# Performance work log

Measured on AMD Instinct MI355X. Metric: run time of the kernel, lower is better.

The kernel has to match this reference:

```python
import jax, jax.numpy as jnp
import numpy as np

B, N, D, H = 8, 8192, 512, 8  # batch, seq, hidden, heads
DH = D // H


def _rope_tables(n, d, dtype=jnp.float32):
    # standard rotate-half RoPE tables over the full hidden dim (d/2 freq pairs)
    half = d // 2
    inv_freq = 1.0 / (10000.0 ** (np.arange(0, half, dtype=np.float32) / half))
    pos = np.arange(n, dtype=np.float32)
    ang = np.einsum('n,f->nf', pos, inv_freq)          # [N, D/2]
    ang = np.concatenate([ang, ang], axis=-1)          # [N, D]
    return jnp.asarray(np.cos(ang), dtype), jnp.asarray(np.sin(ang), dtype)


def setup_inputs() -> dict:
    key = jax.random.key(0)
    k1, k2 = jax.random.split(key)
    hidden_states = jax.random.normal(k1, (B, N, D), dtype=jnp.float32)
    num_layers = 24
    std = 0.02 / np.sqrt(2.0 * num_layers * D)
    W = jax.random.normal(k2, (D, D), dtype=jnp.float32) * std
    cos, sin = _rope_tables(N, D)
    return {"hidden_states": hidden_states, "W": W, "cos": cos, "sin": sin}


def _rotate_half(x):
    x1, x2 = jnp.split(x, 2, axis=-1)
    return jnp.concatenate([-x2, x1], axis=-1)


def reference(hidden_states, W, cos, sin):
    # dropout(p=0) in eval mode -> identity
    x = hidden_states * cos + _rotate_half(hidden_states) * sin  # RoPE, [B,N,D]
    q = jnp.einsum('bnd,ed->bne', x, W)                          # F.linear(x, W)
    qh = q.reshape(B, N, H, DH)
    xh = x.reshape(B, N, H, DH)
    # linear-complexity path: (K^T V) then Q @ (.), per head
    kv = jnp.einsum('bnhd,bnhe->bhde', xh, xh)   # [B,H,DH,DH]
    out = jnp.einsum('bnhd,bhde->bnhe', qh, kv)  # [B,N,H,DH]
    return out.reshape(B, N, D)
```

## Files before the change

### kernel.cpp

```cpp
#include <hip/hip_runtime.h>
#include <hip/hip_bf16.h>
#include <stdint.h>

#define BB 8
#define NN 8192
#define DD 512
#define HH 8
#define DHD 64
#define NCH 32

typedef __attribute__((ext_vector_type(8))) short bf16x8;
typedef __attribute__((ext_vector_type(4))) float f32x4;
typedef __attribute__((ext_vector_type(4))) float f4v;

__device__ __forceinline__ unsigned short f2bf(float f) {
  union { float f; unsigned int u; } v; v.f = f;
  return (unsigned short)((v.u + 0x7FFFu + ((v.u >> 16) & 1u)) >> 16);
}

__device__ __forceinline__ void async16(const void* g, void* l) {
  __builtin_amdgcn_global_load_lds(
      (const __attribute__((address_space(1))) void*)g,
      (__attribute__((address_space(3))) void*)l, 16, 0, 0);
}

__global__ __launch_bounds__(512, 2) void ropekv_kernel(
    const float* __restrict__ h, const float* __restrict__ cs,
    const float* __restrict__ sn, unsigned short* __restrict__ x,
    float* __restrict__ kvp, int nbh) {
  __shared__ __align__(16) unsigned int xt32[512 * 34];
  int blk = blockIdx.x;
  int chunk = blk & 31, b = blk >> 5;
  int tid = threadIdx.x;
  int wave = tid >> 6, lane = tid & 63;
  int rpar = lane & 1;
  int g = lane >> 1;
  int cf = g * 8;
  int l15 = lane & 15, q = lane >> 4;
  int hd = wave * 64;
  size_t row0 = (size_t)b * NN + (size_t)chunk * 256;
  int n0 = chunk * 256;

  f32x4 acc[4][4];
#pragma unroll
  for (int i = 0; i < 4; ++i)
#pragma unroll
    for (int j = 0; j < 4; ++j) acc[i][j] = (f32x4){0.f, 0.f, 0.f, 0.f};

  f4v ha[4][2], hbv[4][2];

  auto loadt = [&](int t) {
#pragma unroll
    for (int p = 0; p < 4; ++p) {
      int r = p * 16 + wave * 2 + rpar;
      const float* hp = h + (row0 + t * 64 + r) * DD + cf;
      ha[p][0]  = __builtin_nontemporal_load((const f4v*)hp);
      ha[p][1]  = __builtin_nontemporal_load((const f4v*)(hp + 4));
      hbv[p][0] = __builtin_nontemporal_load((const f4v*)(hp + 256));
      hbv[p][1] = __builtin_nontemporal_load((const f4v*)(hp + 260));
    }
  };

  auto ropet = [&](int t) {
#pragma unroll
    for (int p = 0; p < 4; ++p) {
      int r = p * 16 + wave * 2 + rpar;
      int nr = n0 + t * 64 + r;
      const float* cp = cs + (size_t)nr * DD + cf;
      const float* sp = sn + (size_t)nr * DD + cf;
      f4v c0 = *(const f4v*)cp, c1 = *(const f4v*)(cp + 4);
      f4v s0 = *(const f4v*)sp, s1 = *(const f4v*)(sp + 4);
      f4v xl0 = ha[p][0] * c0 - hbv[p][0] * s0;
      f4v xl1 = ha[p][1] * c1 - hbv[p][1] * s1;
      f4v xh0 = hbv[p][0] * c0 + ha[p][0] * s0;
      f4v xh1 = hbv[p][1] * c1 + ha[p][1] * s1;
      unsigned ml[4], mh[4];
      ml[0] = (unsigned)f2bf(xl0.x) | ((unsigned)f2bf(xl0.y) << 16);
      ml[1] = (unsigned)f2bf(xl0.z) | ((unsigned)f2bf(xl0.w) << 16);
      ml[2] = (unsigned)f2bf(xl1.x) | ((unsigned)f2bf(xl1.y) << 16);
      ml[3] = (unsigned)f2bf(xl1.z) | ((unsigned)f2bf(xl1.w) << 16);
      mh[0] = (unsigned)f2bf(xh0.x) | ((unsigned)f2bf(xh0.y) << 16);
      mh[1] = (unsigned)f2bf(xh0.z) | ((unsigned)f2bf(xh0.w) << 16);
      mh[2] = (unsigned)f2bf(xh1.x) | ((unsigned)f2bf(xh1.y) << 16);
      mh[3] = (unsigned)f2bf(xh1.z) | ((unsigned)f2bf(xh1.w) << 16);
      unsigned short* xp = x + (row0 + t * 64 + r) * DD + cf;
      uint4 st0; st0.x = ml[0]; st0.y = ml[1]; st0.z = ml[2]; st0.w = ml[3];
      uint4 st1; st1.x = mh[0]; st1.y = mh[1]; st1.z = mh[2]; st1.w = mh[3];
      *(uint4*)xp         = st0;
      *(uint4*)(xp + 256) = st1;
      unsigned pk[8];
#pragma unroll
      for (int k = 0; k < 4; ++k) {
        unsigned mine = rpar ? mh[k] : ml[k];
        unsigned send = rpar ? ml[k] : mh[k];
        unsigned recv = (unsigned)__shfl_xor((int)send, 1, 64);
        if (!rpar) {
          pk[2 * k]     = (mine & 0xffffu) | (recv << 16);
          pk[2 * k + 1] = (mine >> 16) | (recv & 0xffff0000u);
        } else {
          pk[2 * k]     = (recv & 0xffffu) | (mine << 16);
          pk[2 * k + 1] = (recv >> 16) | (mine & 0xffff0000u);
        }
      }
      int np = p * 8 + wave;
      int dbase = cf + (rpar ? 256 : 0);
      int rot = (g >> 1) & 7;
#pragma unroll
      for (int w = 0; w < 8; ++w) {
        int jj = (w + rot) & 7;
        xt32[(dbase + jj) * 34 + np] = pk[jj];
      }
    }
  };

  loadt(0);
  for (int t = 0; t < 4; ++t) {
    ropet(t);
    __syncthreads();
    if (t < 3) loadt(t + 1);
    const unsigned short* xt16 = (const unsigned short*)xt32;
#pragma unroll
    for (int ks = 0; ks < 64; ks += 32) {
      bf16x8 af[4];
#pragma unroll
      for (int i = 0; i < 4; ++i)
        af[i] = *(const bf16x8*)&xt16[(hd + i * 16 + l15) * 68 + ks + q * 8];
#pragma unroll
      for (int i = 0; i < 4; ++i)
#pragma unroll
        for (int j = 0; j < 4; ++j)
          acc[i][j] = __builtin_amdgcn_mfma_f32_16x16x32_bf16(af[i], af[j], acc[i][j], 0, 0, 0);
    }
    __syncthreads();
  }

  int bh = b * 8 + wave;
  float* dst = kvp + ((size_t)chunk * nbh + bh) * 4096;
#pragma unroll
  for (int i = 0; i < 4; ++i)
#pragma unroll
    for (int j = 0; j < 4; ++j)
#pragma unroll
      for (int reg = 0; reg < 4; ++reg)
        dst[(i * 16 + q * 4 + reg) * 64 + j * 16 + l15] = acc[i][j][reg];
}

__global__ __launch_bounds__(512, 2) void wkvt_kernel(
    const float* __restrict__ W, const float* __restrict__ kvp,
    unsigned short* __restrict__ wkvt, int nbh) {
  __shared__ float kvs[64 * 16];
  __shared__ __align__(16) float ws[64 * 512];
  int blk = blockIdx.x;
  int bh = blk >> 2, eq = blk & 3;
  int b = bh >> 3, hh = bh & 7;
  int tid = threadIdx.x;
  if (tid < 256) {
    int idx = tid * 4;
    int d = idx >> 4, ec = idx & 15;
    f4v s = (f4v){0.f, 0.f, 0.f, 0.f};
    for (int c = 0; c < NCH; ++c)
      s += *(const f4v*)&kvp[((size_t)c * nbh + bh) * 4096 + d * 64 + eq * 16 + ec];
    *(f4v*)&kvs[idx] = s;
  }
#pragma unroll
  for (int i = 0; i < 16; ++i) {
    int idx = i * 2048 + tid * 4;
    *(f4v*)&ws[idx] = *(const f4v*)&W[(size_t)(hh * DHD + (idx >> 9)) * DD + (idx & 511)];
  }
  __syncthreads();
  int el = tid & 15, fg = tid >> 4;
  f4v av[4];
#pragma unroll
  for (int k = 0; k < 4; ++k) av[k] = (f4v){0.f, 0.f, 0.f, 0.f};
#pragma unroll 8
  for (int d = 0; d < 64; ++d) {
    float kvv = kvs[d * 16 + el];
    const f4v* wr = (const f4v*)&ws[d * DD + fg * 16];
#pragma unroll
    for (int k = 0; k < 4; ++k) av[k] += wr[k] * kvv;
  }
  unsigned short tb[16];
#pragma unroll
  for (int k = 0; k < 4; ++k) {
    tb[k * 4 + 0] = f2bf(av[k].x); tb[k * 4 + 1] = f2bf(av[k].y);
    tb[k * 4 + 2] = f2bf(av[k].z); tb[k * 4 + 3] = f2bf(av[k].w);
  }
  size_t ob = ((size_t)b * DD + hh * DHD + eq * 16 + el) * DD + fg * 16;
  *(uint4*)&wkvt[ob]     = *(uint4*)&tb[0];
  *(uint4*)&wkvt[ob + 8] = *(uint4*)&tb[8];
}

__global__ __launch_bounds__(256, 2) void gemm_kernel(const unsigned short* __restrict__ x,
                                                      const unsigned short* __restrict__ wkvt,
                                                      float* __restrict__ out) {
  __shared__ __align__(16) unsigned short As[128 * 64];
  __shared__ __align__(16) unsigned short Bs[256 * 64];
  int mt = blockIdx.x, ct = blockIdx.y, bz = blockIdx.z;
  int tid = threadIdx.x, wave = tid >> 6, lane = tid & 63;
  int m_off = (wave & 1) * 64, c_off = (wave >> 1) * 128;
  int l15 = lane & 15, q = lane >> 4;
  int lrow = lane >> 3, lcol = (lane & 7) * 8;
  const unsigned short* Ag = x    + ((size_t)bz * NN + mt * 128) * DD;
  const unsigned short* Bg = wkvt + ((size_t)bz * DD + ct * 256) * DD;
  f32x4 acc[4][8];
#pragma unroll
  for (int i = 0; i < 4; ++i)
#pragma unroll
    for (int j = 0; j < 8; ++j) acc[i][j] = (f32x4){0.f, 0.f, 0.f, 0.f};

  for (int kk = 0; kk < 512; kk += 64) {
#pragma unroll
    for (int i = 0; i < 4; ++i)
      async16(Ag + (size_t)(wave * 32 + i * 8 + lrow) * DD + kk + lcol,
              &As[(wave * 32 + i * 8) * 64]);
#pragma unroll
    for (int i = 0; i < 8; ++i)
      async16(Bg + (size_t)(wave * 64 + i * 8 + lrow) * DD + kk + lcol,
              &Bs[(wave * 64 + i * 8) * 64]);
    __syncthreads();
#pragma unroll
    for (int ks = 0; ks < 64; ks += 32) {
      bf16x8 a[4], bb[8];
#pragma unroll
      for (int i = 0; i < 4; ++i)
        a[i] = *(const bf16x8*)&As[(m_off + i * 16 + l15) * 64 + ks + q * 8];
#pragma unroll
      for (int j = 0; j < 8; ++j)
        bb[j] = *(const bf16x8*)&Bs[(c_off + j * 16 + l15) * 64 + ks + q * 8];
#pragma unroll
      for (int i = 0; i < 4; ++i)
#pragma unroll
        for (int j = 0; j < 8; ++j)
          acc[i][j] = __builtin_amdgcn_mfma_f32_16x16x32_bf16(a[i], bb[j], acc[i][j], 0, 0, 0);
    }
    __syncthreads();
  }
  float* ob = out + ((size_t)bz * NN + mt * 128) * DD + ct * 256;
#pragma unroll
  for (int i = 0; i < 4; ++i)
#pragma unroll
    for (int j = 0; j < 8; ++j) {
      int row = m_off + i * 16 + q * 4;
      int col = c_off + j * 16 + l15;
#pragma unroll
      for (int reg = 0; reg < 4; ++reg)
        __builtin_nontemporal_store(acc[i][j][reg], &ob[(size_t)(row + reg) * DD + col]);
    }
}

extern "C" void kernel_launch(void* const* d_in, const int* in_sizes, int n_in,
                              void* d_out, int out_size, void* d_ws, size_t ws_size,
                              hipStream_t stream) {
  (void)in_sizes; (void)n_in; (void)out_size;
  const float* h  = (const float*)d_in[0];
  const float* W  = (const float*)d_in[1];
  const float* cs = (const float*)d_in[2];
  const float* sn = (const float*)d_in[3];
  float* out = (float*)d_out;

  const size_t x_full     = (size_t)BB * NN * DD * 2;
  const size_t kvp_full   = (size_t)NCH * BB * HH * DHD * DHD * 4;
  const size_t wkvt_full  = (size_t)BB * DD * DD * 2;
  const size_t x_batch    = (size_t)NN * DD * 2;
  const size_t kvp_batch  = (size_t)NCH * HH * DHD * DHD * 4;
  const size_t wkvt_batch = (size_t)DD * DD * 2;

  if (ws_size >= x_full + kvp_full + wkvt_full) {
    unsigned short* xw   = (unsigned short*)d_ws;
    float*          kvp  = (float*)((char*)d_ws + x_full);
    unsigned short* wkvt = (unsigned short*)((char*)d_ws + x_full + kvp_full);
    ropekv_kernel<<<dim3(BB * 32), dim3(512), 0, stream>>>(h, cs, sn, xw, kvp, BB * HH);
    wkvt_kernel<<<dim3(BB * HH * 4), dim3(512), 0, stream>>>(W, kvp, wkvt, BB * HH);
    gemm_kernel<<<dim3(NN / 128, DD / 256, BB), dim3(256), 0, stream>>>(xw, wkvt, out);
  } else {
    unsigned short* xw   = (unsigned short*)d_ws;
    float*          kvp  = (float*)((char*)d_ws + x_batch);
    unsigned short* wkvt = (unsigned short*)((char*)d_ws + x_batch + kvp_batch);
    for (int b = 0; b < BB; ++b) {
      ropekv_kernel<<<dim3(32), dim3(512), 0, stream>>>(
          h + (size_t)b * NN * DD, cs, sn, xw, kvp, HH);
      wkvt_kernel<<<dim3(HH * 4), dim3(512), 0, stream>>>(W, kvp, wkvt, HH);
      gemm_kernel<<<dim3(NN / 128, DD / 256, 1), dim3(256), 0, stream>>>(
          xw, wkvt, out + (size_t)b * NN * DD);
    }
  }
}
```

Measured before the change: 336.0 us.

## Rewrite GEMM as 256x256 tile, 8-wave, double-buffered pipelined kernel

The GEMM kernel moves from 128x256 tiles with 4 waves and a single LDS buffer to 256x256 tiles with 8 waves. LDS is split into double-buffered halves, and async global-to-LDS loads for future k-steps are interleaved with MFMA work using explicit vmcnt waits, barriers and setprio. LDS is XOR-swizzled to avoid bank conflicts, and the 1D grid is remapped to a chiplet-aware block order. The aim is to hide memory latency and improve operand reuse, at the cost of a more fragile hand-scheduled pipeline and lower occupancy from the larger LDS and register footprint.

Result: no change. 331.0 us (-1.5%).

```diff
diff --git a/kernel.cpp b/kernel.cpp
--- a/kernel.cpp
+++ b/kernel.cpp
@@ -190,62 +190,128 @@
   *(uint4*)&wkvt[ob + 8] = *(uint4*)&tb[8];
 }
 
-__global__ __launch_bounds__(256, 2) void gemm_kernel(const unsigned short* __restrict__ x,
+constexpr int c_stM[8] = {0, 1, 0, 1, 0, 1, 0, 1};
+constexpr int c_stP[8] = {1, 1, 0, 0, 0, 0, 1, 1};
+constexpr int c_stH[8] = {1, 1, 0, 0, 1, 1, 0, 0};
+constexpr int c_stO[8] = {1, 1, 2, 2, 2, 2, 3, 3};
+
+__global__ __launch_bounds__(512, 2) void gemm_kernel(const unsigned short* __restrict__ x,
                                                       const unsigned short* __restrict__ wkvt,
                                                       float* __restrict__ out) {
-  __shared__ __align__(16) unsigned short As[128 * 64];
-  __shared__ __align__(16) unsigned short Bs[256 * 64];
-  int mt = blockIdx.x, ct = blockIdx.y, bz = blockIdx.z;
+  __shared__ __align__(16) unsigned short Ab[2][2][128 * 64];
+  __shared__ __align__(16) unsigned short Bb[2][2][128 * 64];
+  int u = blockIdx.x;
+  int cpx = gridDim.x >> 3;
+  int l = (u & 7) * cpx + (u >> 3);
+  int ct = l & 1, mt = (l >> 1) & 31, bz = l >> 6;
   int tid = threadIdx.x, wave = tid >> 6, lane = tid & 63;
-  int m_off = (wave & 1) * 64, c_off = (wave >> 1) * 128;
+  int wm = wave & 1, wn = wave >> 1;
   int l15 = lane & 15, q = lane >> 4;
-  int lrow = lane >> 3, lcol = (lane & 7) * 8;
-  const unsigned short* Ag = x    + ((size_t)bz * NN + mt * 128) * DD;
+  const unsigned short* Ag = x    + ((size_t)bz * NN + mt * 256) * DD;
   const unsigned short* Bg = wkvt + ((size_t)bz * DD + ct * 256) * DD;
-  f32x4 acc[4][8];
-#pragma unroll
-  for (int i = 0; i < 4; ++i)
-#pragma unroll
-    for (int j = 0; j < 8; ++j) acc[i][j] = (f32x4){0.f, 0.f, 0.f, 0.f};
-
-  for (int kk = 0; kk < 512; kk += 64) {
-#pragma unroll
-    for (int i = 0; i < 4; ++i)
-      async16(Ag + (size_t)(wave * 32 + i * 8 + lrow) * DD + kk + lcol,
-              &As[(wave * 32 + i * 8) * 64]);
-#pragma unroll
-    for (int i = 0; i < 8; ++i)
-      async16(Bg + (size_t)(wave * 64 + i * 8 + lrow) * DD + kk + lcol,
-              &Bs[(wave * 64 + i * 8) * 64]);
-    __syncthreads();
-#pragma unroll
-    for (int ks = 0; ks < 64; ks += 32) {
-      bf16x8 a[4], bb[8];
-#pragma unroll
-      for (int i = 0; i < 4; ++i)
-        a[i] = *(const bf16x8*)&As[(m_off + i * 16 + l15) * 64 + ks + q * 8];
-#pragma unroll
-      for (int j = 0; j < 8; ++j)
-        bb[j] = *(const bf16x8*)&Bs[(c_off + j * 16 + l15) * 64 + ks + q * 8];
-#pragma unroll
-      for (int i = 0; i < 4; ++i)
-#pragma unroll
-        for (int j = 0; j < 8; ++j)
-          acc[i][j] = __builtin_amdgcn_mfma_f32_16x16x32_bf16(a[i], bb[j], acc[i][j], 0, 0, 0);
-    }
-    __syncthreads();
-  }
-  float* ob = out + ((size_t)bz * NN + mt * 128) * DD + ct * 256;
-#pragma unroll
-  for (int i = 0; i < 4; ++i)
+
+  int row0 = tid >> 3,         ss0 = (tid & 7) ^ (row0 & 7);
+  int row1 = (512 + tid) >> 3, ss1 = ((512 + tid) & 7) ^ (row1 & 7);
+  const unsigned short* At0 = Ag + (size_t)row0 * DD + ss0 * 8;
+  const unsigned short* At1 = Ag + (size_t)row1 * DD + ss1 * 8;
+  const unsigned short* Bt0 = Bg + (size_t)row0 * DD + ss0 * 8;
+  const unsigned short* Bt1 = Bg + (size_t)row1 * DD + ss1 * 8;
+
+  auto stgA = [&](int P, int hf, int kt) {
+    async16(At0 + (size_t)hf * 128 * DD + kt * 64, &Ab[P][hf][wave * 512]);
+    async16(At1 + (size_t)hf * 128 * DD + kt * 64, &Ab[P][hf][4096 + wave * 512]);
+  };
+  auto stgB = [&](int P, int hf, int kt) {
+    async16(Bt0 + (size_t)hf * 128 * DD + kt * 64, &Bb[P][hf][wave * 512]);
+    async16(Bt1 + (size_t)hf * 128 * DD + kt * 64, &Bb[P][hf][4096 + wave * 512]);
+  };
+
+  int sw0 = ((q ^ (l15 & 7)) << 3);
+  int sw1 = (((4 + q) ^ (l15 & 7)) << 3);
+
+  bf16x8 Ar[4][2], Br[4][2];
+  auto loadA4 = [&](int P, int a) {
+#pragma unroll
+    for (int f = 0; f < 4; ++f) {
+      int r = (a * 64 + f * 16 + l15) * 64;
+      Ar[f][0] = *(const bf16x8*)&Ab[P][wm][r + sw0];
+      Ar[f][1] = *(const bf16x8*)&Ab[P][wm][r + sw1];
+    }
+  };
+  auto loadB2 = [&](int P, int n0) {
+#pragma unroll
+    for (int f = 0; f < 2; ++f) {
+      int r = ((wn & 1) * 64 + (n0 + f) * 16 + l15) * 64;
+      Br[n0 + f][0] = *(const bf16x8*)&Bb[P][wn >> 1][r + sw0];
+      Br[n0 + f][1] = *(const bf16x8*)&Bb[P][wn >> 1][r + sw1];
+    }
+  };
+
+  f32x4 acc[8][4];
+#pragma unroll
+  for (int i = 0; i < 8; ++i)
+#pragma unroll
+    for (int j = 0; j < 4; ++j) acc[i][j] = (f32x4){0.f, 0.f, 0.f, 0.f};
+
+  stgB(0, 0, 0); stgA(0, 0, 0); stgB(0, 1, 0); stgA(0, 1, 0);
+  stgB(1, 0, 1); stgA(1, 0, 1);
+  asm volatile("s_waitcnt vmcnt(4)" ::: "memory");
+  __builtin_amdgcn_s_barrier();
+
+#pragma unroll
+  for (int i = 0; i < 4; ++i) {
 #pragma unroll
     for (int j = 0; j < 8; ++j) {
-      int row = m_off + i * 16 + q * 4;
-      int col = c_off + j * 16 + l15;
-#pragma unroll
-      for (int reg = 0; reg < 4; ++reg)
-        __builtin_nontemporal_store(acc[i][j][reg], &ob[(size_t)(row + reg) * DD + col]);
-    }
+      constexpr int jm[8] = {0, 1, 0, 1, 0, 1, 0, 1};
+      (void)jm;
+      int P = j >> 2;
+      int a = (j >> 1) & 1;
+      int b2 = (j & 1) * 2;
+      if ((j & 3) == 0) loadB2(P, 0);
+      if ((j & 3) == 1) loadB2(P, 2);
+      if ((j & 1) == 0) loadA4(P, a);
+      if (2 * i + c_stO[j] < 8) {
+        if (c_stM[j]) stgA(c_stP[j], c_stH[j], 2 * i + c_stO[j]);
+        else          stgB(c_stP[j], c_stH[j], 2 * i + c_stO[j]);
+      }
+      __builtin_amdgcn_s_barrier();
+      asm volatile("s_waitcnt lgkmcnt(0)" ::: "memory");
+      __builtin_amdgcn_sched_barrier(0);
+      __builtin_amdgcn_s_setprio(1);
+#pragma unroll
+      for (int f = 0; f < 4; ++f)
+#pragma unroll
+        for (int nn = 0; nn < 2; ++nn) {
+          acc[a * 4 + f][b2 + nn] = __builtin_amdgcn_mfma_f32_16x16x32_bf16(
+              Ar[f][0], Br[b2 + nn][0], acc[a * 4 + f][b2 + nn], 0, 0, 0);
+          acc[a * 4 + f][b2 + nn] = __builtin_amdgcn_mfma_f32_16x16x32_bf16(
+              Ar[f][1], Br[b2 + nn][1], acc[a * 4 + f][b2 + nn], 0, 0, 0);
+        }
+      __builtin_amdgcn_s_setprio(0);
+      if (i == 3 && j == 3) {
+        asm volatile("s_waitcnt vmcnt(0)" ::: "memory");
+      } else if ((j & 3) == 3) {
+        asm volatile("s_waitcnt vmcnt(4)" ::: "memory");
+      }
+      __builtin_amdgcn_s_barrier();
+    }
+  }
+
+  float* ob = out + ((size_t)bz * NN + mt * 256 + wm * 128) * DD + ct * 256 + wn * 64;
+#pragma unroll
+  for (int f = 0; f < 4; ++f) {
+#pragma unroll
+    for (int a = 0; a < 2; ++a)
+#pragma unroll
+      for (int nn = 0; nn < 4; ++nn) {
+        int row = a * 64 + f * 16 + q * 4;
+        int col = nn * 16 + l15;
+#pragma unroll
+        for (int reg = 0; reg < 4; ++reg)
+          __builtin_nontemporal_store(acc[a * 4 + f][nn][reg],
+                                      &ob[(size_t)(row + reg) * DD + col]);
+      }
+  }
 }
 
 extern "C" void kernel_launch(void* const* d_in, const int* in_sizes, int n_in,
@@ -271,7 +337,7 @@
     unsigned short* wkvt = (unsigned short*)((char*)d_ws + x_full + kvp_full);
     ropekv_kernel<<<dim3(BB * 32), dim3(512), 0, stream>>>(h, cs, sn, xw, kvp, BB * HH);
     wkvt_kernel<<<dim3(BB * HH * 4), dim3(512), 0, stream>>>(W, kvp, wkvt, BB * HH);
-    gemm_kernel<<<dim3(NN / 128, DD / 256, BB), dim3(256), 0, stream>>>(xw, wkvt, out);
+    gemm_kernel<<<dim3((NN / 256) * (DD / 256) * BB), dim3(512), 0, stream>>>(xw, wkvt, out);
   } else {
     unsigned short* xw   = (unsigned short*)d_ws;
     float*          kvp  = (float*)((char*)d_ws + x_batch);
@@ -280,7 +346,7 @@
       ropekv_kernel<<<dim3(32), dim3(512), 0, stream>>>(
           h + (size_t)b * NN * DD, cs, sn, xw, kvp, HH);
       wkvt_kernel<<<dim3(HH * 4), dim3(512), 0, stream>>>(W, kvp, wkvt, HH);
-      gemm_kernel<<<dim3(NN / 128, DD / 256, 1), dim3(256), 0, stream>>>(
+      gemm_kernel<<<dim3((NN / 256) * (DD / 256)), dim3(512), 0, stream>>>(
           xw, wkvt, out + (size_t)b * NN * DD);
     }
   }
```

## Double-buffer LDS tile and register prefetch in RoPE/KV kernel pipeline

Applied to the files above, without the earlier changes.

The kernel now keeps two LDS transpose buffers and two register sets for the loaded hidden-state tiles. The loop is software-pipelined: loads run two tiles ahead and RoPE runs one tile ahead of the MFMA accumulation, which drops one barrier per iteration. The aim is to overlap global loads and RoPE ALU work with the matrix ops. In exchange, LDS per block roughly doubles (about 139KB), which may not fit two blocks per CU. The extra register buffers also raise register pressure under launch_bounds(512,2).

New measurement: 336.0 us. About the same (+0.0%).

```diff
diff --git a/kernel.cpp b/kernel.cpp
--- a/kernel.cpp
+++ b/kernel.cpp
@@ -28,7 +28,7 @@
     const float* __restrict__ h, const float* __restrict__ cs,
     const float* __restrict__ sn, unsigned short* __restrict__ x,
     float* __restrict__ kvp, int nbh) {
-  __shared__ __align__(16) unsigned int xt32[512 * 34];
+  __shared__ __align__(16) unsigned int xt32[2][512 * 34];
   int blk = blockIdx.x;
   int chunk = blk & 31, b = blk >> 5;
   int tid = threadIdx.x;
@@ -47,21 +47,23 @@
 #pragma unroll
     for (int j = 0; j < 4; ++j) acc[i][j] = (f32x4){0.f, 0.f, 0.f, 0.f};
 
-  f4v ha[4][2], hbv[4][2];
+  f4v ha[2][4][2], hb[2][4][2];
 
   auto loadt = [&](int t) {
+    int pb = t & 1;
 #pragma unroll
     for (int p = 0; p < 4; ++p) {
       int r = p * 16 + wave * 2 + rpar;
       const float* hp = h + (row0 + t * 64 + r) * DD + cf;
-      ha[p][0]  = __builtin_nontemporal_load((const f4v*)hp);
-      ha[p][1]  = __builtin_nontemporal_load((const f4v*)(hp + 4));
-      hbv[p][0] = __builtin_nontemporal_load((const f4v*)(hp + 256));
-      hbv[p][1] = __builtin_nontemporal_load((const f4v*)(hp + 260));
+      ha[pb][p][0] = __builtin_nontemporal_load((const f4v*)hp);
+      ha[pb][p][1] = __builtin_nontemporal_load((const f4v*)(hp + 4));
+      hb[pb][p][0] = __builtin_nontemporal_load((const f4v*)(hp + 256));
+      hb[pb][p][1] = __builtin_nontemporal_load((const f4v*)(hp + 260));
     }
   };
 
   auto ropet = [&](int t) {
+    int pb = t & 1;
 #pragma unroll
     for (int p = 0; p < 4; ++p) {
       int r = p * 16 + wave * 2 + rpar;
@@ -70,10 +72,10 @@
       const float* sp = sn + (size_t)nr * DD + cf;
       f4v c0 = *(const f4v*)cp, c1 = *(const f4v*)(cp + 4);
       f4v s0 = *(const f4v*)sp, s1 = *(const f4v*)(sp + 4);
-      f4v xl0 = ha[p][0] * c0 - hbv[p][0] * s0;
-      f4v xl1 = ha[p][1] * c1 - hbv[p][1] * s1;
-      f4v xh0 = hbv[p][0] * c0 + ha[p][0] * s0;
-      f4v xh1 = hbv[p][1] * c1 + ha[p][1] * s1;
+      f4v xl0 = ha[pb][p][0] * c0 - hb[pb][p][0] * s0;
+      f4v xl1 = ha[pb][p][1] * c1 - hb[pb][p][1] * s1;
+      f4v xh0 = hb[pb][p][0] * c0 + ha[pb][p][0] * s0;
+      f4v xh1 = hb[pb][p][1] * c1 + ha[pb][p][1] * s1;
       unsigned ml[4], mh[4];
       ml[0] = (unsigned)f2bf(xl0.x) | ((unsigned)f2bf(xl0.y) << 16);
       ml[1] = (unsigned)f2bf(xl0.z) | ((unsigned)f2bf(xl0.w) << 16);
@@ -108,17 +110,13 @@
 #pragma unroll
       for (int w = 0; w < 8; ++w) {
         int jj = (w + rot) & 7;
-        xt32[(dbase + jj) * 34 + np] = pk[jj];
+        xt32[pb][(dbase + jj) * 34 + np] = pk[jj];
       }
     }
   };
 
-  loadt(0);
-  for (int t = 0; t < 4; ++t) {
-    ropet(t);
-    __syncthreads();
-    if (t < 3) loadt(t + 1);
-    const unsigned short* xt16 = (const unsigned short*)xt32;
+  auto mfmat = [&](int t) {
+    const unsigned short* xt16 = (const unsigned short*)xt32[t & 1];
 #pragma unroll
     for (int ks = 0; ks < 64; ks += 32) {
       bf16x8 af[4];
@@ -131,6 +129,17 @@
         for (int j = 0; j < 4; ++j)
           acc[i][j] = __builtin_amdgcn_mfma_f32_16x16x32_bf16(af[i], af[j], acc[i][j], 0, 0, 0);
     }
+  };
+
+  loadt(0);
+  ropet(0);
+  loadt(1);
+  __syncthreads();
+#pragma unroll
+  for (int t = 0; t < 4; ++t) {
+    if (t < 2) loadt(t + 2);
+    if (t < 3) ropet(t + 1);
+    mfmat(t);
     __syncthreads();
   }
 
```
